# Optimization experiments

Measured on AMD Instinct MI355X. Metric: run time of the kernel, lower is better.

Reference implementation:

```python
import jax, jax.numpy as jnp
import numpy as np

N, E, DIN, DH, NG, DOUT = 65536, 524288, 128, 128, 256, 3
EPS = 1e-5  # torch BatchNorm1d default


def setup_inputs():
    key = jax.random.key(0)
    ks = jax.random.split(key, 32)

    def p(k, shape, s=0.05):
        return jax.random.normal(k, shape, jnp.float32) * s

    inp = {
        "x": jax.random.normal(ks[0], (N, DIN), jnp.float32),
        "edge_index": jax.random.randint(ks[1], (2, E), 0, N),
        "batch": jnp.sort(jax.random.randint(ks[2], (N,), 0, NG)),
    }
    # live GATv2 layers: gat1 128->128, gat2 128->64, gat3 64->32 (gat4 output is
    # overwritten by h4 = dropout(h3) in the source, so gat4/m4 are dead code)
    dims = [(DIN, 128), (128, 64), (64, 32)]
    i = 3
    for l, (di, do) in enumerate(dims, start=1):
        inp[f"g{l}_Wl"] = p(ks[i], (di, do)); i += 1
        inp[f"g{l}_bl"] = jnp.zeros((do,), jnp.float32)
        inp[f"g{l}_Wr"] = p(ks[i], (di, do)); i += 1
        inp[f"g{l}_br"] = jnp.zeros((do,), jnp.float32)
        inp[f"g{l}_att"] = p(ks[i], (do,)); i += 1
        inp[f"g{l}_b"] = jnp.zeros((do,), jnp.float32)
        inp[f"bn{l}_g"] = jnp.ones((do,), jnp.float32)
        inp[f"bn{l}_b"] = jnp.zeros((do,), jnp.float32)
    inp["lin1_W"] = p(ks[i], (256, 128)); i += 1
    inp["lin1_b"] = jnp.zeros((128,), jnp.float32)
    inp["bn5_g"] = jnp.ones((128,), jnp.float32)
    inp["bn5_b"] = jnp.zeros((128,), jnp.float32)
    inp["lin2_W"] = p(ks[i], (128, DOUT)); i += 1
    inp["lin2_b"] = jnp.zeros((DOUT,), jnp.float32)
    inp["train"] = 0  # dropout disabled (eval)
    return inp


def _bn(h, g, b):
    # BatchNorm1d with batch statistics (biased variance, as torch normalizes)
    mu = h.mean(0)
    var = h.var(0)
    return g * (h - mu) * jax.lax.rsqrt(var + EPS) + b


def _gatv2(x, src, dst, Wl, bl, Wr, br, att, b, n):
    xl = x @ Wl + bl  # [N, C] source-side transform (also the message value)
    xr = x @ Wr + br  # [N, C] target-side transform
    e = jax.nn.leaky_relu(xl[src] + xr[dst], 0.2) @ att  # [E] attention logits
    m = jax.ops.segment_max(e, dst, num_segments=n)      # segment softmax over in-edges
    ex = jnp.exp(e - m[dst])
    alpha = ex / jax.ops.segment_sum(ex, dst, num_segments=n)[dst]
    return jax.ops.segment_sum(alpha[:, None] * xl[src], dst, num_segments=n) + b


def reference(x, edge_index, batch,
              g1_Wl, g1_bl, g1_Wr, g1_br, g1_att, g1_b, bn1_g, bn1_b,
              g2_Wl, g2_bl, g2_Wr, g2_br, g2_att, g2_b, bn2_g, bn2_b,
              g3_Wl, g3_bl, g3_Wr, g3_br, g3_att, g3_b, bn3_g, bn3_b,
              lin1_W, lin1_b, bn5_g, bn5_b, lin2_W, lin2_b, train):
    loops = jnp.arange(N)
    src = jnp.concatenate([edge_index[0], loops])  # PyG add_self_loops=True
    dst = jnp.concatenate([edge_index[1], loops])

    h1 = _bn(jax.nn.relu(_gatv2(x,  src, dst, g1_Wl, g1_bl, g1_Wr, g1_br, g1_att, g1_b, N)), bn1_g, bn1_b)
    h2 = _bn(jax.nn.relu(_gatv2(h1, src, dst, g2_Wl, g2_bl, g2_Wr, g2_br, g2_att, g2_b, N)), bn2_g, bn2_b)
    h3 = _bn(jax.nn.relu(_gatv2(h2, src, dst, g3_Wl, g3_bl, g3_Wr, g3_br, g3_att, g3_b, N)), bn3_g, bn3_b)

    p1 = jax.ops.segment_sum(h1, batch, num_segments=NG)  # global_add_pool
    p2 = jax.ops.segment_sum(h2, batch, num_segments=NG)
    p3 = jax.ops.segment_sum(h3, batch, num_segments=NG)
    # source overwrites h4 = dropout(h3), so the fourth pooled block is h3 again
    h = jnp.concatenate([p1, p2, p3, p3], axis=1)  # [NG, 256]

    h = _bn(jax.nn.relu(h @ lin1_W + lin1_b), bn5_g, bn5_b)
    h = h @ lin2_W + lin2_b
    return (jax.nn.sigmoid(h), jax.nn.log_softmax(h, axis=1))
```

## Files before the change

### kernel.cpp

```cpp
#include <hip/hip_runtime.h>
#include <math.h>
#include <type_traits>

#define NN 65536
#define NE 524288
#define NT (NN + NE)
#define NG 256
#define BN_EPS 1e-5f
#define NSLOT 64

typedef __attribute__((ext_vector_type(8))) __bf16 bf16x8;
typedef __attribute__((ext_vector_type(4))) float f32x4;

__device__ inline unsigned pk2(float lo, float hi) {
    unsigned a = (unsigned)__builtin_bit_cast(unsigned short, (__bf16)lo);
    unsigned b = (unsigned)__builtin_bit_cast(unsigned short, (__bf16)hi);
    return a | (b << 16);
}
__device__ inline void bf2(unsigned u, float& a, float& b) {
    a = __uint_as_float(u << 16);
    b = __uint_as_float(u & 0xFFFF0000u);
}
__device__ inline void unpk(uint4 u, float* v) {
    bf2(u.x, v[0], v[1]); bf2(u.y, v[2], v[3]);
    bf2(u.z, v[4], v[5]); bf2(u.w, v[6], v[7]);
}
__device__ inline void unpk(uint2 u, float* v) {
    bf2(u.x, v[0], v[1]); bf2(u.y, v[2], v[3]);
}
__device__ inline void unpk(unsigned u, float* v) { bf2(u, v[0], v[1]); }


__global__ __launch_bounds__(256) void k_pre(
        const int* __restrict__ ei, int* __restrict__ counts,
        const float* __restrict__ W1l, const float* __restrict__ W1r,
        const float* __restrict__ W2l, const float* __restrict__ W2r,
        const float* __restrict__ W3l, const float* __restrict__ W3r,
        unsigned short* __restrict__ f1l, unsigned short* __restrict__ f1r,
        unsigned short* __restrict__ f2l, unsigned short* __restrict__ f2r,
        unsigned short* __restrict__ f3l, unsigned short* __restrict__ f3r) {
    if (blockIdx.x < 2048) {
        int i = blockIdx.x * 256 + threadIdx.x;
        atomicAdd(&counts[ei[NE + i]], 1);
        return;
    }
    int idx = (blockIdx.x - 2048) * 256 + threadIdx.x;
    const float* W; unsigned short* Wf; int DO, base;
    if (idx < 2048)      { W = W1l; Wf = f1l; DO = 128; base = 0; }
    else if (idx < 4096) { W = W1r; Wf = f1r; DO = 128; base = 2048; }
    else if (idx < 5120) { W = W2l; Wf = f2l; DO = 64;  base = 4096; }
    else if (idx < 6144) { W = W2r; Wf = f2r; DO = 64;  base = 5120; }
    else if (idx < 6400) { W = W3l; Wf = f3l; DO = 32;  base = 6144; }
    else                 { W = W3r; Wf = f3r; DO = 32;  base = 6400; }
    int li = idx - base;
    int lane = li & 63;
    int fr = li >> 6;
    int nf = fr % (DO / 16);
    int kk = fr / (DO / 16);
    int k0 = kk * 32 + (lane >> 4) * 8;
    int c = nf * 16 + (lane & 15);
    unsigned short o[8];
#pragma unroll
    for (int j = 0; j < 8; ++j)
        o[j] = __builtin_bit_cast(unsigned short, (__bf16)W[(size_t)(k0 + j) * DO + c]);
    uint4 p;
    p.x = o[0] | ((unsigned)o[1] << 16);
    p.y = o[2] | ((unsigned)o[3] << 16);
    p.z = o[4] | ((unsigned)o[5] << 16);
    p.w = o[6] | ((unsigned)o[7] << 16);
    ((uint4*)(Wf))[li] = p;
}


__global__ void k_scanA(const int* __restrict__ counts, int* __restrict__ bsum) {
    __shared__ int l[256];
    int t = threadIdx.x;
    int v = counts[blockIdx.x * 256 + t] + 1;
    l[t] = v;
    __syncthreads();
    for (int st = 128; st > 0; st >>= 1) {
        if (t < st) l[t] += l[t + st];
        __syncthreads();
    }
    if (t == 0) bsum[blockIdx.x] = l[0];
}


__global__ void k_scanBC(const int* __restrict__ counts, const int* __restrict__ bsum,
                         int* __restrict__ off, int* __restrict__ wofs) {
    __shared__ int lb[256];
    __shared__ int l[256];
    int t = threadIdx.x;
    int bv = bsum[t];
    lb[t] = bv;
    __syncthreads();
    for (int d = 1; d < 256; d <<= 1) {
        int u = (t >= d) ? lb[t - d] : 0;
        __syncthreads();
        lb[t] += u;
        __syncthreads();
    }
    int boffv = lb[blockIdx.x] - bsum[blockIdx.x];
    int i = blockIdx.x * 256 + t;
    int v = counts[i] + 1;
    l[t] = v;
    __syncthreads();
    for (int d = 1; d < 256; d <<= 1) {
        int u = (t >= d) ? l[t - d] : 0;
        __syncthreads();
        l[t] += u;
        __syncthreads();
    }
    int e = boffv + l[t] - v;
    off[i] = e;
    wofs[i] = e;
    if (i == 0) off[NN] = NT;
}


__global__ __launch_bounds__(256) void k_scatter(
        const int* __restrict__ ei, const int* __restrict__ batch,
        int* __restrict__ wofs, int* __restrict__ csr_src,
        int* __restrict__ gstart, int* __restrict__ gend) {
    int base = blockIdx.x * 1024 + threadIdx.x;
    int srcv[4], posv[4];
#pragma unroll
    for (int k = 0; k < 4; ++k) {
        int i = base + k * 256;
        if (i < NN) {
            int b = batch[i];
            if (i == 0) gstart[b] = 0;
            if (i == NN - 1) gend[b] = NN;
            else {
                int b2 = batch[i + 1];
                if (b2 != b) { gend[b] = i + 1; gstart[b2] = i + 1; }
            }
        }
        int src, dst;
        if (i < NE) { src = ei[i]; dst = ei[NE + i]; }
        else        { src = dst = i - NE; }
        srcv[k] = src;
        posv[k] = atomicAdd(&wofs[dst], 1);
    }
#pragma unroll
    for (int k = 0; k < 4; ++k) csr_src[posv[k]] = srcv[k];
}


template <int DI, int DO, bool BN>
__global__ __launch_bounds__(256) void k_gemm2m(
        const float* __restrict__ x,
        const unsigned short* __restrict__ Wfl, const unsigned short* __restrict__ Wfr,
        const float* __restrict__ bl, const float* __restrict__ br,
        const float* __restrict__ stats, const float* __restrict__ bg,
        const float* __restrict__ bb,
        unsigned short* __restrict__ xl, unsigned short* __restrict__ xr) {
    constexpr int NF = DO / 16;
    constexpr int NK = DI / 32;
    const int lane = threadIdx.x & 63;
    const int wid = threadIdx.x >> 6;
    const int lg = lane >> 4, ll = lane & 15;
    const int nbase = blockIdx.x * 128 + wid * 32;

    __shared__ float sbn[BN ? 2 * DI : 2];
    float* ssc = sbn;
    float* ssh = sbn + (BN ? DI : 1);
    if constexpr (BN) {
        int t = threadIdx.x;
        if (t < DI) {
            float s = 0.f, q = 0.f;
            for (int k = 0; k < NSLOT; ++k) {
                s += stats[k * 2 * DI + t];
                q += stats[k * 2 * DI + DI + t];
            }
            float mean = s * (1.f / NN);
            float var = q * (1.f / NN) - mean * mean;
            float sc = bg[t] * rsqrtf(var + BN_EPS);
            ssc[t] = sc;
            ssh[t] = bb[t] - mean * sc;
        }
        __syncthreads();
    }

    f32x4 acc[2][NF][2] = {};

    for (int kk = 0; kk < NK; ++kk) {
        const int k0 = kk * 32 + lg * 8;
        float4 sca, scb, sha, shb;
        if constexpr (BN) {
            sca = *(const float4*)(ssc + k0);
            scb = *(const float4*)(ssc + k0 + 4);
            sha = *(const float4*)(ssh + k0);
            shb = *(const float4*)(ssh + k0 + 4);
        }
        bf16x8 xa[2];
#pragma unroll
        for (int nm = 0; nm < 2; ++nm) {
            const float* xp = x + (size_t)(nbase + nm * 16 + ll) * DI + k0;
            float4 v0 = *(const float4*)xp;
            float4 v1 = *(const float4*)(xp + 4);
            if constexpr (BN) {
                v0.x = v0.x * sca.x + sha.x;
                v0.y = v0.y * sca.y + sha.y;
                v0.z = v0.z * sca.z + sha.z;
                v0.w = v0.w * sca.w + sha.w;
                v1.x = v1.x * scb.x + shb.x;
                v1.y = v1.y * scb.y + shb.y;
                v1.z = v1.z * scb.z + shb.z;
                v1.w = v1.w * scb.w + shb.w;
            }
            bf16x8 t;
            t[0] = (__bf16)v0.x; t[1] = (__bf16)v0.y;
            t[2] = (__bf16)v0.z; t[3] = (__bf16)v0.w;
            t[4] = (__bf16)v1.x; t[5] = (__bf16)v1.y;
            t[6] = (__bf16)v1.z; t[7] = (__bf16)v1.w;
            xa[nm] = t;
        }
        const unsigned short* wlp = Wfl + ((size_t)(kk * NF) * 64 + lane) * 8;
        const unsigned short* wrp = Wfr + ((size_t)(kk * NF) * 64 + lane) * 8;
#pragma unroll
        for (int nf = 0; nf < NF; ++nf) {
            bf16x8 wl = __builtin_bit_cast(bf16x8, *(const uint4*)(wlp + (size_t)nf * 64 * 8));
            bf16x8 wr = __builtin_bit_cast(bf16x8, *(const uint4*)(wrp + (size_t)nf * 64 * 8));
#pragma unroll
            for (int nm = 0; nm < 2; ++nm) {
                acc[nm][nf][0] = __builtin_amdgcn_mfma_f32_16x16x32_bf16(wl, xa[nm], acc[nm][nf][0], 0, 0, 0);
                acc[nm][nf][1] = __builtin_amdgcn_mfma_f32_16x16x32_bf16(wr, xa[nm], acc[nm][nf][1], 0, 0, 0);
            }
        }
    }

#pragma unroll
    for (int nf = 0; nf < NF; ++nf) {
        float4 blv = *(const float4*)(bl + nf * 16 + lg * 4);
        float4 brv = *(const float4*)(br + nf * 16 + lg * 4);
#pragma unroll
        for (int nm = 0; nm < 2; ++nm) {
            size_t base = (size_t)(nbase + nm * 16 + ll) * DO + nf * 16 + lg * 4;
            f32x4 a = acc[nm][nf][0];
            uint2 p;
            p.x = pk2(a[0] + blv.x, a[1] + blv.y);
            p.y = pk2(a[2] + blv.z, a[3] + blv.w);
            *(uint2*)(xl + base) = p;
            f32x4 r = acc[nm][nf][1];
            uint2 q;
            q.x = pk2(r[0] + brv.x, r[1] + brv.y);
            q.y = pk2(r[2] + brv.z, r[3] + brv.w);
            *(uint2*)(xr + base) = q;
        }
    }
}


template <int DO, bool WRITEH, int PBASE>
__global__ __launch_bounds__(256) void k_agg8(
        const unsigned short* __restrict__ xl, const unsigned short* __restrict__ xr,
        const int* __restrict__ off, const int* __restrict__ srcs,
        const float* __restrict__ att, const float* __restrict__ bias,
        const int* __restrict__ batch,
        float* __restrict__ out, float* __restrict__ statbuf,
        float* __restrict__ rawpool) {
    constexpr int CPL = DO / 16;
    using UT = typename std::conditional<CPL == 8, uint4,
               typename std::conditional<CPL == 4, uint2, unsigned>::type>::type;
    int wid = threadIdx.x >> 6;
    int lane = threadIdx.x & 63;
    int sg = lane >> 4;
    int sl = lane & 15;
    int cbase = sl * CPL;

    __shared__ float sO[16][DO];
    __shared__ int gb[16];
    if (threadIdx.x < 16) gb[threadIdx.x] = batch[blockIdx.x * 16 + threadIdx.x];

    float atv[CPL];
    if constexpr (CPL == 8) {
        float4 a0 = ((const float4*)att)[sl * 2], a1 = ((const float4*)att)[sl * 2 + 1];
        atv[0] = a0.x; atv[1] = a0.y; atv[2] = a0.z; atv[3] = a0.w;
        atv[4] = a1.x; atv[5] = a1.y; atv[6] = a1.z; atv[7] = a1.w;
    } else if constexpr (CPL == 4) {
        float4 a0 = ((const float4*)att)[sl];
        atv[0] = a0.x; atv[1] = a0.y; atv[2] = a0.z; atv[3] = a0.w;
    } else {
        float2 a0 = ((const float2*)att)[sl];
        atv[0] = a0.x; atv[1] = a0.y;
    }

    int nb = blockIdx.x * 16 + wid * 4;
    for (int n = 0; n < 4; ++n) {
        int node = nb + n;
        float xrv[CPL];
        unpk(*(const UT*)(xr + (size_t)node * DO + cbase), xrv);
        float spart = 0.f;
        float acc[CPL] = {};
        int e0 = off[node], e1 = off[node + 1];

        int jp = e0 + sg;
        bool actp = (jp < e1);
        int srcp = srcs[actp ? jp : e1 - 1];
        UT up = *(const UT*)(xl + (size_t)srcp * DO + cbase);

        for (int jb = e0; jb < e1; jb += 4) {
            UT u = up;
            bool act = actp;
            if (jb + 4 < e1) {
                int jn = jb + 4 + sg;
                actp = (jn < e1);
                int srcn = srcs[actp ? jn : e1 - 1];
                up = *(const UT*)(xl + (size_t)srcn * DO + cbase);
            }
            float v[CPL];
            unpk(u, v);
            float pd = 0.f;
#pragma unroll
            for (int i = 0; i < CPL; ++i) {
                float t = v[i] + xrv[i];
                t = fmaxf(t, 0.2f * t);
                pd = fmaf(t, atv[i], pd);
            }
#pragma unroll
            for (int d = 1; d < 16; d <<= 1) pd += __shfl_xor(pd, d);
            float w = act ? __expf(pd) : 0.f;
            spart += w;
#pragma unroll
            for (int i = 0; i < CPL; ++i) acc[i] = fmaf(w, v[i], acc[i]);
        }
        spart += __shfl_xor(spart, 16);
        spart += __shfl_xor(spart, 32);
#pragma unroll
        for (int i = 0; i < CPL; ++i) {
            acc[i] += __shfl_xor(acc[i], 16);
            acc[i] += __shfl_xor(acc[i], 32);
        }
        if (sg == 0) {
            float inv = 1.f / spart;
            float o[CPL];
#pragma unroll
            for (int i = 0; i < CPL; ++i) {
                o[i] = fmaxf(acc[i] * inv + bias[cbase + i], 0.f);
                sO[wid * 4 + n][cbase + i] = o[i];
            }
            if constexpr (WRITEH) {
                if constexpr (CPL == 8) {
                    float4 oa = {o[0], o[1], o[2], o[3]}, ob = {o[4], o[5], o[6], o[7]};
                    ((float4*)out)[(size_t)node * 32 + sl * 2] = oa;
                    ((float4*)out)[(size_t)node * 32 + sl * 2 + 1] = ob;
                } else if constexpr (CPL == 4) {
                    float4 oa = {o[0], o[1], o[2], o[3]};
                    ((float4*)out)[(size_t)node * 16 + sl] = oa;
                } else {
                    float2 oa = {o[0], o[1]};
                    ((float2*)out)[(size_t)node * 16 + sl] = oa;
                }
            }
        }
    }
    __syncthreads();
    int t = threadIdx.x;
    if (t < DO) {
        float pa = sO[0][t];
        float s = pa, q = pa * pa;
        int cg = gb[0];
#pragma unroll
        for (int w = 1; w < 16; ++w) {
            float vw = sO[w][t];
            s += vw;
            q += vw * vw;
            int g = gb[w];
            if (g != cg) {
                atomicAdd(&rawpool[(size_t)cg * 224 + PBASE + t], pa);
                pa = 0.f;
                cg = g;
            }
            pa += vw;
        }
        atomicAdd(&rawpool[(size_t)cg * 224 + PBASE + t], pa);
        float* sb = statbuf + (size_t)(blockIdx.x & (NSLOT - 1)) * 2 * DO;
        atomicAdd(&sb[t], s);
        atomicAdd(&sb[DO + t], q);
    }
}


__global__ __launch_bounds__(128) void k_head1(
        const float* __restrict__ rawpool,
        const int* __restrict__ gstart, const int* __restrict__ gend,
        const float* __restrict__ st1, const float* __restrict__ st2,
        const float* __restrict__ st3,
        const float* __restrict__ g1, const float* __restrict__ b1,
        const float* __restrict__ g2, const float* __restrict__ b2,
        const float* __restrict__ g3, const float* __restrict__ b3,
        const float* __restrict__ W1, const float* __restrict__ b1l,
        float* __restrict__ z) {
    __shared__ float row[256];
    int g = blockIdx.x, c = threadIdx.x;
    float cnt = (float)(gend[g] - gstart[g]);
    {
        float s = 0.f, q = 0.f;
        for (int k = 0; k < NSLOT; ++k) {
            s += st1[k * 256 + c];
            q += st1[k * 256 + 128 + c];
        }
        float mean = s * (1.f / NN);
        float var = q * (1.f / NN) - mean * mean;
        float sc = g1[c] * rsqrtf(var + BN_EPS);
        float sh = b1[c] - mean * sc;
        row[c] = sc * rawpool[(size_t)g * 224 + c] + sh * cnt;
    }
    {
        float sc, sh, rv;
        if (c < 64) {
            float s = 0.f, q = 0.f;
            for (int k = 0; k < NSLOT; ++k) {
                s += st2[k * 128 + c];
                q += st2[k * 128 + 64 + c];
            }
            float mean = s * (1.f / NN);
            float var = q * (1.f / NN) - mean * mean;
            sc = g2[c] * rsqrtf(var + BN_EPS);
            sh = b2[c] - mean * sc;
            rv = rawpool[(size_t)g * 224 + 128 + c];
        } else {
            int j = (c < 96) ? c - 64 : c - 96;
            float s = 0.f, q = 0.f;
            for (int k = 0; k < NSLOT; ++k) {
                s += st3[k * 64 + j];
                q += st3[k * 64 + 32 + j];
            }
            float mean = s * (1.f / NN);
            float var = q * (1.f / NN) - mean * mean;
            sc = g3[j] * rsqrtf(var + BN_EPS);
            sh = b3[j] - mean * sc;
            rv = rawpool[(size_t)g * 224 + 192 + j];
        }
        row[128 + c] = sc * rv + sh * cnt;
    }
    __syncthreads();
    float acc = b1l[c];
#pragma unroll 16
    for (int k = 0; k < 256; ++k) acc += row[k] * W1[k * 128 + c];
    z[g * 128 + c] = acc > 0.f ? acc : 0.f;
}

__global__ void k_head2(const float* __restrict__ z, const float* __restrict__ g5,
                        const float* __restrict__ b5, const float* __restrict__ W2,
                        const float* __restrict__ b2, float* __restrict__ out) {
    __shared__ float row[128];
    __shared__ float lg[3];
    int g = blockIdx.x, t = threadIdx.x;
    double s = 0.0, q = 0.0;
    for (int gg = 0; gg < NG; ++gg) {
        float v = z[gg * 128 + t];
        s += v;
        q += (double)v * v;
    }
    double mean = s * (1.0 / NG);
    double var = q * (1.0 / NG) - mean * mean;
    float sc = g5[t] * rsqrtf((float)var + BN_EPS);
    float sh = b5[t] - (float)mean * sc;
    row[t] = z[g * 128 + t] * sc + sh;
    __syncthreads();
    if (t < 3) {
        float acc = b2[t];
        for (int k = 0; k < 128; ++k) acc += row[k] * W2[k * 3 + t];
        lg[t] = acc;
    }
    __syncthreads();
    if (t == 0) {
        float l0 = lg[0], l1 = lg[1], l2 = lg[2];
        float mx = fmaxf(l0, fmaxf(l1, l2));
        float lse = mx + logf(expf(l0 - mx) + expf(l1 - mx) + expf(l2 - mx));
        out[g * 3 + 0] = 1.f / (1.f + expf(-l0));
        out[g * 3 + 1] = 1.f / (1.f + expf(-l1));
        out[g * 3 + 2] = 1.f / (1.f + expf(-l2));
        out[NG * 3 + g * 3 + 0] = l0 - lse;
        out[NG * 3 + g * 3 + 1] = l1 - lse;
        out[NG * 3 + g * 3 + 2] = l2 - lse;
    }
}


extern "C" void kernel_launch(void* const* d_in, const int* in_sizes, int n_in,
                              void* d_out, int out_size, void* d_ws, size_t ws_size,
                              hipStream_t stream) {
    const float* x   = (const float*)d_in[0];
    const int* ei    = (const int*)d_in[1];
    const int* batch = (const int*)d_in[2];
    auto F = [&](int i) { return (const float*)d_in[i]; };

    char* ws = (char*)d_ws;
    size_t o = 0;
    auto alloc = [&](size_t bytes) {
        char* p = ws + o;
        o += (bytes + 255) & ~(size_t)255;
        return p;
    };
    int* csr_off  = (int*)alloc((NN + 1) * 4);
    int* wofs     = (int*)alloc(NN * 4);
    int* bsum     = (int*)alloc(256 * 4);
    int* csr_src  = (int*)alloc((size_t)NT * 4);
    unsigned short* xl = (unsigned short*)alloc((size_t)NN * 128 * 2);
    unsigned short* xr = (unsigned short*)alloc((size_t)NN * 128 * 2);
    float* h1     = (float*)alloc((size_t)NN * 128 * 4);
    float* h2     = (float*)alloc((size_t)NN * 64 * 4);
    float* z      = (float*)alloc(NG * 128 * 4);
    size_t zbytes = (size_t)NN * 4 + (size_t)NSLOT * (256 + 128 + 64) * 4 +
                    (size_t)NG * 224 * 4 + 2 * NG * 4;
    char* zchunk  = alloc(zbytes);
    int* counts   = (int*)zchunk;
    float* stat1  = (float*)(zchunk + (size_t)NN * 4);
    float* stat2  = stat1 + NSLOT * 256;
    float* stat3  = stat2 + NSLOT * 128;
    float* rawpool = stat3 + NSLOT * 64;
    int* gstart   = (int*)(rawpool + (size_t)NG * 224);
    int* gend     = gstart + NG;
    unsigned short* wfl1 = (unsigned short*)alloc(128 * 128 * 2);
    unsigned short* wfr1 = (unsigned short*)alloc(128 * 128 * 2);
    unsigned short* wfl2 = (unsigned short*)alloc(128 * 64 * 2);
    unsigned short* wfr2 = (unsigned short*)alloc(128 * 64 * 2);
    unsigned short* wfl3 = (unsigned short*)alloc(64 * 32 * 2);
    unsigned short* wfr3 = (unsigned short*)alloc(64 * 32 * 2);

    hipMemsetAsync(zchunk, 0, zbytes, stream);

    k_pre<<<2048 + 26, 256, 0, stream>>>(ei, counts,
                                         F(3), F(5), F(11), F(13), F(19), F(21),
                                         wfl1, wfr1, wfl2, wfr2, wfl3, wfr3);
    k_scanA<<<NN / 256, 256, 0, stream>>>(counts, bsum);
    k_scanBC<<<NN / 256, 256, 0, stream>>>(counts, bsum, csr_off, wofs);
    k_scatter<<<NT / 1024, 256, 0, stream>>>(ei, batch, wofs, csr_src,
                                             gstart, gend);

    k_gemm2m<128, 128, false><<<NN / 128, 256, 0, stream>>>(
        x, wfl1, wfr1, F(4), F(6), nullptr, nullptr, nullptr, xl, xr);
    k_agg8<128, true, 0><<<NN / 16, 256, 0, stream>>>(
        xl, xr, csr_off, csr_src, F(7), F(8), batch, h1, stat1, rawpool);

    k_gemm2m<128, 64, true><<<NN / 128, 256, 0, stream>>>(
        h1, wfl2, wfr2, F(12), F(14), stat1, F(9), F(10), xl, xr);
    k_agg8<64, true, 128><<<NN / 16, 256, 0, stream>>>(
        xl, xr, csr_off, csr_src, F(15), F(16), batch, h2, stat2, rawpool);

    k_gemm2m<64, 32, true><<<NN / 128, 256, 0, stream>>>(
        h2, wfl3, wfr3, F(20), F(22), stat2, F(17), F(18), xl, xr);
    k_agg8<32, false, 192><<<NN / 16, 256, 0, stream>>>(
        xl, xr, csr_off, csr_src, F(23), F(24), batch, nullptr, stat3, rawpool);

    k_head1<<<NG, 128, 0, stream>>>(rawpool, gstart, gend, stat1, stat2, stat3,
                                    F(9), F(10), F(17), F(18), F(25), F(26),
                                    F(27), F(28), z);
    k_head2<<<NG, 128, 0, stream>>>(z, F(29), F(30), F(31), F(32), (float*)d_out);
}
```

Measured before the change: 243.0 us.

## Store hidden activations in bf16 and use single-wave aggregation blocks

Intermediate layer outputs h1/h2 are written as packed bf16 instead of fp32, and the GEMM kernel is templated to read bf16 input, halving activation traffic. The aggregation kernel now runs one wave per block over 4 nodes, accumulating pooling and BN statistics in registers instead of a shared-memory reduction with a block barrier. This increases the total number of global atomics and adds bf16 rounding to activations before batch norm statistics use.

After: 468.2 us. 1.93x slower.

```diff
diff --git a/kernel.cpp b/kernel.cpp
--- a/kernel.cpp
+++ b/kernel.cpp
@@ -147,9 +147,9 @@
 }
 
 
-template <int DI, int DO, bool BN>
+template <int DI, int DO, bool BN, typename XT>
 __global__ __launch_bounds__(256) void k_gemm2m(
-        const float* __restrict__ x,
+        const XT* __restrict__ x,
         const unsigned short* __restrict__ Wfl, const unsigned short* __restrict__ Wfr,
         const float* __restrict__ bl, const float* __restrict__ br,
         const float* __restrict__ stats, const float* __restrict__ bg,
@@ -196,24 +196,30 @@
         bf16x8 xa[2];
 #pragma unroll
         for (int nm = 0; nm < 2; ++nm) {
-            const float* xp = x + (size_t)(nbase + nm * 16 + ll) * DI + k0;
-            float4 v0 = *(const float4*)xp;
-            float4 v1 = *(const float4*)(xp + 4);
+            float w[8];
+            if constexpr (std::is_same<XT, float>::value) {
+                const float* xp = x + (size_t)(nbase + nm * 16 + ll) * DI + k0;
+                float4 v0 = *(const float4*)xp;
+                float4 v1 = *(const float4*)(xp + 4);
+                w[0] = v0.x; w[1] = v0.y; w[2] = v0.z; w[3] = v0.w;
+                w[4] = v1.x; w[5] = v1.y; w[6] = v1.z; w[7] = v1.w;
+            } else {
+                const unsigned short* xp = x + (size_t)(nbase + nm * 16 + ll) * DI + k0;
+                unpk(*(const uint4*)xp, w);
+            }
             if constexpr (BN) {
-                v0.x = v0.x * sca.x + sha.x;
-                v0.y = v0.y * sca.y + sha.y;
-                v0.z = v0.z * sca.z + sha.z;
-                v0.w = v0.w * sca.w + sha.w;
-                v1.x = v1.x * scb.x + shb.x;
-                v1.y = v1.y * scb.y + shb.y;
-                v1.z = v1.z * scb.z + shb.z;
-                v1.w = v1.w * scb.w + shb.w;
+                w[0] = w[0] * sca.x + sha.x;
+                w[1] = w[1] * sca.y + sha.y;
+                w[2] = w[2] * sca.z + sha.z;
+                w[3] = w[3] * sca.w + sha.w;
+                w[4] = w[4] * scb.x + shb.x;
+                w[5] = w[5] * scb.y + shb.y;
+                w[6] = w[6] * scb.z + shb.z;
+                w[7] = w[7] * scb.w + shb.w;
             }
             bf16x8 t;
-            t[0] = (__bf16)v0.x; t[1] = (__bf16)v0.y;
-            t[2] = (__bf16)v0.z; t[3] = (__bf16)v0.w;
-            t[4] = (__bf16)v1.x; t[5] = (__bf16)v1.y;
-            t[6] = (__bf16)v1.z; t[7] = (__bf16)v1.w;
+#pragma unroll
+            for (int j = 0; j < 8; ++j) t[j] = (__bf16)w[j];
             xa[nm] = t;
         }
         const unsigned short* wlp = Wfl + ((size_t)(kk * NF) * 64 + lane) * 8;
@@ -253,25 +259,20 @@
 
 
 template <int DO, bool WRITEH, int PBASE>
-__global__ __launch_bounds__(256) void k_agg8(
+__global__ __launch_bounds__(64) void k_agg9(
         const unsigned short* __restrict__ xl, const unsigned short* __restrict__ xr,
         const int* __restrict__ off, const int* __restrict__ srcs,
         const float* __restrict__ att, const float* __restrict__ bias,
         const int* __restrict__ batch,
-        float* __restrict__ out, float* __restrict__ statbuf,
+        unsigned short* __restrict__ hout, float* __restrict__ statbuf,
         float* __restrict__ rawpool) {
     constexpr int CPL = DO / 16;
     using UT = typename std::conditional<CPL == 8, uint4,
                typename std::conditional<CPL == 4, uint2, unsigned>::type>::type;
-    int wid = threadIdx.x >> 6;
-    int lane = threadIdx.x & 63;
+    int lane = threadIdx.x;
     int sg = lane >> 4;
     int sl = lane & 15;
     int cbase = sl * CPL;
-
-    __shared__ float sO[16][DO];
-    __shared__ int gb[16];
-    if (threadIdx.x < 16) gb[threadIdx.x] = batch[blockIdx.x * 16 + threadIdx.x];
 
     float atv[CPL];
     if constexpr (CPL == 8) {
@@ -285,8 +286,14 @@
         float2 a0 = ((const float2*)att)[sl];
         atv[0] = a0.x; atv[1] = a0.y;
     }
-
-    int nb = blockIdx.x * 16 + wid * 4;
+    float bi[CPL];
+#pragma unroll
+    for (int i = 0; i < CPL; ++i) bi[i] = bias[cbase + i];
+
+    float ps[CPL] = {}, qs[CPL] = {}, pp[CPL] = {};
+    int nb = blockIdx.x * 4;
+    int cg = batch[nb];
+
     for (int n = 0; n < 4; ++n) {
         int node = nb + n;
         float xrv[CPL];
@@ -336,48 +343,47 @@
             float inv = 1.f / spart;
             float o[CPL];
 #pragma unroll
+            for (int i = 0; i < CPL; ++i)
+                o[i] = fmaxf(fmaf(acc[i], inv, bi[i]), 0.f);
+            int g = batch[node];
+            if (g != cg) {
+#pragma unroll
+                for (int i = 0; i < CPL; ++i) {
+                    atomicAdd(&rawpool[(size_t)cg * 224 + PBASE + cbase + i], pp[i]);
+                    pp[i] = 0.f;
+                }
+                cg = g;
+            }
+#pragma unroll
             for (int i = 0; i < CPL; ++i) {
-                o[i] = fmaxf(acc[i] * inv + bias[cbase + i], 0.f);
-                sO[wid * 4 + n][cbase + i] = o[i];
+                pp[i] += o[i];
+                ps[i] += o[i];
+                qs[i] += o[i] * o[i];
             }
             if constexpr (WRITEH) {
                 if constexpr (CPL == 8) {
-                    float4 oa = {o[0], o[1], o[2], o[3]}, ob = {o[4], o[5], o[6], o[7]};
-                    ((float4*)out)[(size_t)node * 32 + sl * 2] = oa;
-                    ((float4*)out)[(size_t)node * 32 + sl * 2 + 1] = ob;
+                    uint4 pkd;
+                    pkd.x = pk2(o[0], o[1]); pkd.y = pk2(o[2], o[3]);
+                    pkd.z = pk2(o[4], o[5]); pkd.w = pk2(o[6], o[7]);
+                    *(uint4*)(hout + (size_t)node * DO + cbase) = pkd;
                 } else if constexpr (CPL == 4) {
-                    float4 oa = {o[0], o[1], o[2], o[3]};
-                    ((float4*)out)[(size_t)node * 16 + sl] = oa;
+                    uint2 pkd;
+                    pkd.x = pk2(o[0], o[1]); pkd.y = pk2(o[2], o[3]);
+                    *(uint2*)(hout + (size_t)node * DO + cbase) = pkd;
                 } else {
-                    float2 oa = {o[0], o[1]};
-                    ((float2*)out)[(size_t)node * 16 + sl] = oa;
+                    *(unsigned*)(hout + (size_t)node * DO + cbase) = pk2(o[0], o[1]);
                 }
             }
         }
     }
-    __syncthreads();
-    int t = threadIdx.x;
-    if (t < DO) {
-        float pa = sO[0][t];
-        float s = pa, q = pa * pa;
-        int cg = gb[0];
-#pragma unroll
-        for (int w = 1; w < 16; ++w) {
-            float vw = sO[w][t];
-            s += vw;
-            q += vw * vw;
-            int g = gb[w];
-            if (g != cg) {
-                atomicAdd(&rawpool[(size_t)cg * 224 + PBASE + t], pa);
-                pa = 0.f;
-                cg = g;
-            }
-            pa += vw;
-        }
-        atomicAdd(&rawpool[(size_t)cg * 224 + PBASE + t], pa);
+    if (sg == 0) {
         float* sb = statbuf + (size_t)(blockIdx.x & (NSLOT - 1)) * 2 * DO;
-        atomicAdd(&sb[t], s);
-        atomicAdd(&sb[DO + t], q);
+#pragma unroll
+        for (int i = 0; i < CPL; ++i) {
+            atomicAdd(&rawpool[(size_t)cg * 224 + PBASE + cbase + i], pp[i]);
+            atomicAdd(&sb[cbase + i], ps[i]);
+            atomicAdd(&sb[DO + cbase + i], qs[i]);
+        }
     }
 }
 
@@ -501,8 +507,8 @@
     int* csr_src  = (int*)alloc((size_t)NT * 4);
     unsigned short* xl = (unsigned short*)alloc((size_t)NN * 128 * 2);
     unsigned short* xr = (unsigned short*)alloc((size_t)NN * 128 * 2);
-    float* h1     = (float*)alloc((size_t)NN * 128 * 4);
-    float* h2     = (float*)alloc((size_t)NN * 64 * 4);
+    unsigned short* h1 = (unsigned short*)alloc((size_t)NN * 128 * 2);
+    unsigned short* h2 = (unsigned short*)alloc((size_t)NN * 64 * 2);
     float* z      = (float*)alloc(NG * 128 * 4);
     size_t zbytes = (size_t)NN * 4 + (size_t)NSLOT * (256 + 128 + 64) * 4 +
                     (size_t)NG * 224 * 4 + 2 * NG * 4;
@@ -531,19 +537,19 @@
     k_scatter<<<NT / 1024, 256, 0, stream>>>(ei, batch, wofs, csr_src,
                                              gstart, gend);
 
-    k_gemm2m<128, 128, false><<<NN / 128, 256, 0, stream>>>(
+    k_gemm2m<128, 128, false, float><<<NN / 128, 256, 0, stream>>>(
         x, wfl1, wfr1, F(4), F(6), nullptr, nullptr, nullptr, xl, xr);
-    k_agg8<128, true, 0><<<NN / 16, 256, 0, stream>>>(
+    k_agg9<128, true, 0><<<NN / 4, 64, 0, stream>>>(
         xl, xr, csr_off, csr_src, F(7), F(8), batch, h1, stat1, rawpool);
 
-    k_gemm2m<128, 64, true><<<NN / 128, 256, 0, stream>>>(
+    k_gemm2m<128, 64, true, unsigned short><<<NN / 128, 256, 0, stream>>>(
         h1, wfl2, wfr2, F(12), F(14), stat1, F(9), F(10), xl, xr);
-    k_agg8<64, true, 128><<<NN / 16, 256, 0, stream>>>(
+    k_agg9<64, true, 128><<<NN / 4, 64, 0, stream>>>(
         xl, xr, csr_off, csr_src, F(15), F(16), batch, h2, stat2, rawpool);
 
-    k_gemm2m<64, 32, true><<<NN / 128, 256, 0, stream>>>(
+    k_gemm2m<64, 32, true, unsigned short><<<NN / 128, 256, 0, stream>>>(
         h2, wfl3, wfr3, F(20), F(22), stat2, F(17), F(18), xl, xr);
-    k_agg8<32, false, 192><<<NN / 16, 256, 0, stream>>>(
+    k_agg9<32, false, 192><<<NN / 4, 64, 0, stream>>>(
         xl, xr, csr_off, csr_src, F(23), F(24), batch, nullptr, stat3, rawpool);
 
     k_head1<<<NG, 128, 0, stream>>>(rawpool, gstart, gend, stat1, stat2, stat3,
```
